# Kernel tuning notes

Hardware: AMD Instinct MI355X
Metric: run time of the kernel (lower is better)

Reference implementation:

```python
import jax, jax.numpy as jnp
import numpy as np

TOP_K = 1
N_EXPERTS = 32
ALPHA = 0.001
SCALING = 1.0


def setup_inputs() -> dict:
    key = jax.random.key(0)
    k1, k2 = jax.random.split(key)
    hidden_states = jax.random.normal(k1, (16, 8192, 256), dtype=jnp.float32)
    # kaiming_uniform-ish gate weight, scale irrelevant for correctness check
    weight = jax.random.normal(k2, (32, 256), dtype=jnp.float32) * 0.06
    return {"hidden_states": hidden_states, "weight": weight}


def reference(hidden_states, weight):
    bsz, seq_len, h = hidden_states.shape
    x = hidden_states.reshape(-1, h).astype(jnp.float32)           # [N, h]
    logits = jnp.einsum('nh,eh->ne', x, weight.astype(jnp.float32))  # [N, E]
    scores = jax.nn.softmax(logits, axis=-1)
    # greedy top-k (sorted order fine; torch uses sorted=False but values identical for k=1)
    topk_weight, topk_idx = jax.lax.top_k(scores, TOP_K)            # [N, K]
    topk_weight = topk_weight * SCALING  # norm_topk_prob=False, top_k=1
    # seq_aux loss (training branch, alpha > 0)
    idx_aux = topk_idx.reshape(bsz, seq_len * TOP_K)                # [B, S*K]
    ce = jax.vmap(lambda idx: jnp.zeros((N_EXPERTS,), jnp.float32).at[idx].add(1.0))(idx_aux)
    ce = ce / (seq_len * TOP_K / N_EXPERTS)
    scores_seq = scores.reshape(bsz, seq_len, N_EXPERTS)
    aux_loss = jnp.mean(jnp.sum(ce * jnp.mean(scores_seq, axis=1), axis=1)) * ALPHA
    return topk_idx, topk_weight, aux_loss
```

## Files before the change

### kernel.cpp

```cpp
#include <hip/hip_runtime.h>
#include <math.h>

#define NTOK (16 * 8192)
#define H    256
#define E    32
#define SEQ  8192
#define BSZ  16

__global__ __launch_bounds__(256) void zero_ws_kernel(float* ws) {
    int i = blockIdx.x * 256 + threadIdx.x;
    if (i < BSZ * E * 2) ws[i] = 0.0f;
}

__global__ __launch_bounds__(256, 2) void gate_kernel(
    const float* __restrict__ x, const float* __restrict__ w,
    float* __restrict__ out, float* __restrict__ ws_cnt, float* __restrict__ ws_sum)
{
    __shared__ float w_lds[E * H];

    const int tid   = threadIdx.x;
    const int token = blockIdx.x * 256 + tid;
    const int lane  = tid & 63;

    {
        float4*       wl = (float4*)w_lds;
        const float4* wg = (const float4*)w;
#pragma unroll
        for (int i = 0; i < (E * H / 4) / 256; ++i)
            wl[tid + 256 * i] = wg[tid + 256 * i];
    }
    __syncthreads();

    float acc[E];
#pragma unroll
    for (int e = 0; e < E; ++e) acc[e] = 0.0f;

    const float* xrow = x + (size_t)token * H;

    float4 cur[4], nxt[4];
#pragma unroll
    for (int j = 0; j < 4; ++j)
        cur[j] = *(const float4*)(xrow + 4 * j);

#pragma unroll 1
    for (int h = 0; h < H; h += 16) {
        const int hn = (h + 16) & (H - 1);
#pragma unroll
        for (int j = 0; j < 4; ++j)
            nxt[j] = *(const float4*)(xrow + hn + 4 * j);

#pragma unroll
        for (int e = 0; e < E; ++e) {
            const float4* wp = (const float4*)(w_lds + e * H + h);
            float s = 0.0f;
#pragma unroll
            for (int j = 0; j < 4; ++j) {
                float4 wv = wp[j];
                s += cur[j].x * wv.x + cur[j].y * wv.y + cur[j].z * wv.z + cur[j].w * wv.w;
            }
            acc[e] += s;
        }
#pragma unroll
        for (int j = 0; j < 4; ++j) cur[j] = nxt[j];
    }

    float m = acc[0];
    int   idx = 0;
#pragma unroll
    for (int e = 1; e < E; ++e) {
        if (acc[e] > m) { m = acc[e]; idx = e; }
    }
    float sc[E];
    float ssum = 0.0f;
#pragma unroll
    for (int e = 0; e < E; ++e) {
        sc[e] = expf(acc[e] - m);
        ssum += sc[e];
    }
    const float inv = 1.0f / ssum;

    out[token]        = (float)idx;
    out[NTOK + token] = inv;

    const int b = token / SEQ;

#pragma unroll 1
    for (int e = 0; e < E; ++e) {
        unsigned long long ball = __ballot(idx == e);
        if (lane == 0 && ball)
            atomicAdd(&ws_cnt[b * E + e], (float)__popcll(ball));
        float v = sc[e] * inv;
#pragma unroll
        for (int off = 32; off > 0; off >>= 1)
            v += __shfl_xor(v, off, 64);
        if (lane == 0)
            atomicAdd(&ws_sum[b * E + e], v);
    }
}

__global__ __launch_bounds__(256) void aux_kernel(
    const float* __restrict__ ws_cnt, const float* __restrict__ ws_sum,
    float* __restrict__ out)
{
    const int tid = threadIdx.x;
    float p = 0.0f;
    for (int i = tid; i < BSZ * E; i += 256)
        p += ws_cnt[i] * ws_sum[i];

    __shared__ float red[4];
#pragma unroll
    for (int off = 32; off > 0; off >>= 1)
        p += __shfl_xor(p, off, 64);
    if ((tid & 63) == 0) red[tid >> 6] = p;
    __syncthreads();
    if (tid == 0) {
        float t = red[0] + red[1] + red[2] + red[3];
        out[2 * NTOK] = t * (0.001f / (16.0f * 256.0f * 8192.0f));
    }
}

extern "C" void kernel_launch(void* const* d_in, const int* in_sizes, int n_in,
                              void* d_out, int out_size, void* d_ws, size_t ws_size,
                              hipStream_t stream) {
    const float* x = (const float*)d_in[0];
    const float* w = (const float*)d_in[1];
    float* out    = (float*)d_out;
    float* ws     = (float*)d_ws;
    float* ws_cnt = ws;
    float* ws_sum = ws + BSZ * E;

    zero_ws_kernel<<<4, 256, 0, stream>>>(ws);
    gate_kernel<<<NTOK / 256, 256, 0, stream>>>(x, w, out, ws_cnt, ws_sum);
    aux_kernel<<<1, 256, 0, stream>>>(ws_cnt, ws_sum, out);
}
```

Before: 284.9 us.

## Compute four tokens per thread with split-K halves to reuse LDS weights

Each thread now accumulates logits for 4 tokens over half of the hidden dimension, so every weight float4 read from LDS is reused across 4 tokens instead of one. The two halves of a wave are combined with a cross-lane shuffle. Each half-lane then finishes softmax and argmax for 2 tokens, and the count and score reductions are merged into one shuffle loop. Blocks shrink to 128 threads while each still covers 256 tokens. The aim is to cut LDS bandwidth per FMA, at the cost of a 128-entry accumulator that raises register pressure and less coalesced global loads, since each lane reads rows spaced H apart.

New measurement: 272.7 us. -4.3%, faster.

```diff
diff --git a/kernel.cpp b/kernel.cpp
--- a/kernel.cpp
+++ b/kernel.cpp
@@ -6,95 +6,116 @@
 #define E    32
 #define SEQ  8192
 #define BSZ  16
+#define T    4
 
 __global__ __launch_bounds__(256) void zero_ws_kernel(float* ws) {
     int i = blockIdx.x * 256 + threadIdx.x;
     if (i < BSZ * E * 2) ws[i] = 0.0f;
 }
 
-__global__ __launch_bounds__(256, 2) void gate_kernel(
+__global__ __launch_bounds__(128, 2) void gate_kernel(
     const float* __restrict__ x, const float* __restrict__ w,
     float* __restrict__ out, float* __restrict__ ws_cnt, float* __restrict__ ws_sum)
 {
     __shared__ float w_lds[E * H];
 
-    const int tid   = threadIdx.x;
-    const int token = blockIdx.x * 256 + tid;
-    const int lane  = tid & 63;
+    const int tid = threadIdx.x;
 
     {
         float4*       wl = (float4*)w_lds;
         const float4* wg = (const float4*)w;
 #pragma unroll
-        for (int i = 0; i < (E * H / 4) / 256; ++i)
-            wl[tid + 256 * i] = wg[tid + 256 * i];
+        for (int i = 0; i < (E * H / 4) / 128; ++i)
+            wl[tid + 128 * i] = wg[tid + 128 * i];
     }
     __syncthreads();
 
-    float acc[E];
+    const int lane = tid & 63;
+    const int col  = lane & 31;
+    const int half = lane >> 5;
+    const int wavebase = blockIdx.x * 256 + (tid >> 6) * 128;
+    const int tok0 = wavebase + col * T;
+
+    const float* xbase = x + (size_t)tok0 * H + half * 128;
+
+    float acc[E][T];
 #pragma unroll
-    for (int e = 0; e < E; ++e) acc[e] = 0.0f;
+    for (int e = 0; e < E; ++e)
+#pragma unroll
+        for (int t = 0; t < T; ++t) acc[e][t] = 0.0f;
 
-    const float* xrow = x + (size_t)token * H;
-
-    float4 cur[4], nxt[4];
+    float4 cur[T], nxt[T];
 #pragma unroll
-    for (int j = 0; j < 4; ++j)
-        cur[j] = *(const float4*)(xrow + 4 * j);
+    for (int t = 0; t < T; ++t)
+        cur[t] = *(const float4*)(xbase + t * H);
 
 #pragma unroll 1
-    for (int h = 0; h < H; h += 16) {
-        const int hn = (h + 16) & (H - 1);
+    for (int hc = 0; hc < 128; hc += 4) {
+        const int hn = (hc + 4) & 127;
 #pragma unroll
-        for (int j = 0; j < 4; ++j)
-            nxt[j] = *(const float4*)(xrow + hn + 4 * j);
+        for (int t = 0; t < T; ++t)
+            nxt[t] = *(const float4*)(xbase + t * H + hn);
 
 #pragma unroll
         for (int e = 0; e < E; ++e) {
-            const float4* wp = (const float4*)(w_lds + e * H + h);
-            float s = 0.0f;
+            const float4 wv = *(const float4*)(w_lds + e * H + half * 128 + hc);
 #pragma unroll
-            for (int j = 0; j < 4; ++j) {
-                float4 wv = wp[j];
-                s += cur[j].x * wv.x + cur[j].y * wv.y + cur[j].z * wv.z + cur[j].w * wv.w;
+            for (int t = 0; t < T; ++t) {
+                acc[e][t] += wv.x * cur[t].x + wv.y * cur[t].y
+                           + wv.z * cur[t].z + wv.w * cur[t].w;
             }
-            acc[e] += s;
         }
 #pragma unroll
-        for (int j = 0; j < 4; ++j) cur[j] = nxt[j];
+        for (int t = 0; t < T; ++t) cur[t] = nxt[t];
     }
 
-    float m = acc[0];
-    int   idx = 0;
 #pragma unroll
-    for (int e = 1; e < E; ++e) {
-        if (acc[e] > m) { m = acc[e]; idx = e; }
+    for (int e = 0; e < E; ++e)
+#pragma unroll
+        for (int t = 0; t < T; ++t)
+            acc[e][t] += __shfl_xor(acc[e][t], 32, 64);
+
+    float m_s[2], inv_s[2];
+    int   idx_s[2];
+#pragma unroll
+    for (int s = 0; s < 2; ++s) {
+        float m = half ? acc[0][2 + s] : acc[0][s];
+        int   id = 0;
+#pragma unroll
+        for (int e = 1; e < E; ++e) {
+            const float v = half ? acc[e][2 + s] : acc[e][s];
+            if (v > m) { m = v; id = e; }
+        }
+        float ss = 0.0f;
+#pragma unroll
+        for (int e = 0; e < E; ++e) {
+            const float v = half ? acc[e][2 + s] : acc[e][s];
+            ss += expf(v - m);
+        }
+        const float inv = 1.0f / ss;
+        const int token = tok0 + half * 2 + s;
+        out[token]        = (float)id;
+        out[NTOK + token] = inv;
+        m_s[s] = m; inv_s[s] = inv; idx_s[s] = id;
     }
-    float sc[E];
-    float ssum = 0.0f;
-#pragma unroll
-    for (int e = 0; e < E; ++e) {
-        sc[e] = expf(acc[e] - m);
-        ssum += sc[e];
-    }
-    const float inv = 1.0f / ssum;
 
-    out[token]        = (float)idx;
-    out[NTOK + token] = inv;
-
-    const int b = token / SEQ;
+    const int b = wavebase >> 13;
 
 #pragma unroll 1
     for (int e = 0; e < E; ++e) {
-        unsigned long long ball = __ballot(idx == e);
-        if (lane == 0 && ball)
-            atomicAdd(&ws_cnt[b * E + e], (float)__popcll(ball));
-        float v = sc[e] * inv;
+        const float v0 = half ? acc[e][2] : acc[e][0];
+        const float v1 = half ? acc[e][3] : acc[e][1];
+        float sc = expf(v0 - m_s[0]) * inv_s[0] + expf(v1 - m_s[1]) * inv_s[1];
+        float cn = (float)((idx_s[0] == e) + (idx_s[1] == e));
 #pragma unroll
-        for (int off = 32; off > 0; off >>= 1)
-            v += __shfl_xor(v, off, 64);
-        if (lane == 0)
-            atomicAdd(&ws_sum[b * E + e], v);
+        for (int off = 32; off > 0; off >>= 1) {
+            sc += __shfl_xor(sc, off, 64);
+            cn += __shfl_xor(cn, off, 64);
+        }
+        if (lane == 0) {
+            atomicAdd(&ws_sum[b * E + e], sc);
+            if (cn != 0.0f) atomicAdd(&ws_cnt[b * E + e], cn);
+        }
     }
 }
 
@@ -130,6 +151,6 @@
     float* ws_sum = ws + BSZ * E;
 
     zero_ws_kernel<<<4, 256, 0, stream>>>(ws);
-    gate_kernel<<<NTOK / 256, 256, 0, stream>>>(x, w, out, ws_cnt, ws_sum);
+    gate_kernel<<<NTOK / 256, 128, 0, stream>>>(x, w, out, ws_cnt, ws_sum);
     aux_kernel<<<1, 256, 0, stream>>>(ws_cnt, ws_sum, out);
 }
```

## Retile gate GEMM into 64-token blocks with LDS-staged x and register tiles

Applied to the files above, without the earlier changes.

Each block now handles 64 tokens instead of 256. Threads split the work across expert groups (8 experts per wave) and hidden-dimension quarters, with x chunks staged through double-buffered LDS and a 4x8 register tile per thread. The softmax max and sum are combined across waves through LDS, and the counts and score sums are reduced with shuffles plus atomics. The aim is fewer per-thread strided row reads, better coalescing and more reuse of weight loads, at the cost of extra syncs, more atomics per token and the 32 KB weight reload now happening in four times as many blocks.

Measured after the change: 297.0 us. +4.2%, slower.

```diff
diff --git a/kernel.cpp b/kernel.cpp
--- a/kernel.cpp
+++ b/kernel.cpp
@@ -6,95 +6,140 @@
 #define E    32
 #define SEQ  8192
 #define BSZ  16
+#define TOKB 64
+#define NCH  16
 
 __global__ __launch_bounds__(256) void zero_ws_kernel(float* ws) {
     int i = blockIdx.x * 256 + threadIdx.x;
     if (i < BSZ * E * 2) ws[i] = 0.0f;
 }
 
-__global__ __launch_bounds__(256, 2) void gate_kernel(
+__global__ __launch_bounds__(256, 4) void gate_kernel(
     const float* __restrict__ x, const float* __restrict__ w,
     float* __restrict__ out, float* __restrict__ ws_cnt, float* __restrict__ ws_sum)
 {
-    __shared__ float w_lds[E * H];
+    __shared__ float  w_lds[E * H];
+    __shared__ float4 xb4[2][256];
 
-    const int tid   = threadIdx.x;
-    const int token = blockIdx.x * 256 + tid;
-    const int lane  = tid & 63;
+    const int tid  = threadIdx.x;
+    const int lane = tid & 63;
+    const int eg   = tid >> 6;
+    const int tg   = lane & 15;
+    const int hq   = lane >> 4;
+
+    const int blkbase = blockIdx.x * TOKB;
 
     {
+        const float4* wg = (const float4*)w;
         float4*       wl = (float4*)w_lds;
-        const float4* wg = (const float4*)w;
 #pragma unroll
-        for (int i = 0; i < (E * H / 4) / 256; ++i)
-            wl[tid + 256 * i] = wg[tid + 256 * i];
+        for (int i = 0; i < 8; ++i) wl[tid + 256 * i] = wg[tid + 256 * i];
+    }
+
+    const int s_tok = tid >> 2, s_part = tid & 3;
+    const float* gsrc = x + (size_t)(blkbase + s_tok) * H + s_part * 4;
+    float4 v = *(const float4*)gsrc;
+
+    float acc[4][8];
+#pragma unroll
+    for (int t = 0; t < 4; ++t)
+#pragma unroll
+        for (int e = 0; e < 8; ++e) acc[t][e] = 0.0f;
+
+#pragma unroll 1
+    for (int kc = 0; kc < NCH; ++kc) {
+        xb4[kc & 1][tid] = v;
+        if (kc < NCH - 1) v = *(const float4*)(gsrc + (kc + 1) * 16);
+        __syncthreads();
+
+        const float* xc = (const float*)xb4[kc & 1];
+        float4 xf[4];
+#pragma unroll
+        for (int t = 0; t < 4; ++t)
+            xf[t] = *(const float4*)(xc + (tg * 4 + t) * 16 + hq * 4);
+
+#pragma unroll
+        for (int e = 0; e < 8; ++e) {
+            const float4 wf = *(const float4*)(w_lds + (eg * 8 + e) * H + kc * 16 + hq * 4);
+#pragma unroll
+            for (int t = 0; t < 4; ++t)
+                acc[t][e] += wf.x * xf[t].x + wf.y * xf[t].y
+                           + wf.z * xf[t].z + wf.w * xf[t].w;
+        }
     }
     __syncthreads();
 
-    float acc[E];
 #pragma unroll
-    for (int e = 0; e < E; ++e) acc[e] = 0.0f;
+    for (int t = 0; t < 4; ++t)
+#pragma unroll
+        for (int e = 0; e < 8; ++e) {
+            acc[t][e] += __shfl_xor(acc[t][e], 16, 64);
+            acc[t][e] += __shfl_xor(acc[t][e], 32, 64);
+        }
 
-    const float* xrow = x + (size_t)token * H;
+    const int etok = tg * 4 + hq;
+    float l[8];
+#pragma unroll
+    for (int e = 0; e < 8; ++e)
+        l[e] = hq == 0 ? acc[0][e] : (hq == 1 ? acc[1][e] : (hq == 2 ? acc[2][e] : acc[3][e]));
 
-    float4 cur[4], nxt[4];
+    float m8 = l[0];
+    int   i8 = 0;
 #pragma unroll
-    for (int j = 0; j < 4; ++j)
-        cur[j] = *(const float4*)(xrow + 4 * j);
+    for (int e = 1; e < 8; ++e)
+        if (l[e] > m8) { m8 = l[e]; i8 = e; }
+    float s8 = 0.0f;
+#pragma unroll
+    for (int e = 0; e < 8; ++e) s8 += expf(l[e] - m8);
 
+    float4* pm = (float4*)xb4;
+    float2* mi = (float2*)((float*)xb4 + 1024);
+    pm[eg * 64 + etok] = make_float4(m8, s8, (float)(eg * 8 + i8), 0.0f);
+    __syncthreads();
+
+    if (tid < 64) {
+        const int tok = tid;
+        float4 p[4];
+#pragma unroll
+        for (int g = 0; g < 4; ++g) p[g] = pm[g * 64 + tok];
+
+        float M = p[0].x, idxf = p[0].z;
+#pragma unroll
+        for (int g = 1; g < 4; ++g)
+            if (p[g].x > M) { M = p[g].x; idxf = p[g].z; }
+        float S = 0.0f;
+#pragma unroll
+        for (int g = 0; g < 4; ++g) S += p[g].y * expf(p[g].x - M);
+        const float inv = 1.0f / S;
+
+        const int T = blkbase + tok;
+        out[T]        = idxf;
+        out[NTOK + T] = inv;
+        mi[tok] = make_float2(M, inv);
+
+        const int IDX = (int)idxf;
+        const int b   = T >> 13;
 #pragma unroll 1
-    for (int h = 0; h < H; h += 16) {
-        const int hn = (h + 16) & (H - 1);
+        for (int e = 0; e < E; ++e) {
+            unsigned long long ball = __ballot(IDX == e);
+            if (lane == 0 && ball)
+                atomicAdd(&ws_cnt[b * E + e], (float)__popcll(ball));
+        }
+    }
+    __syncthreads();
+
+    {
+        const float2 p = mi[etok];
+        const int b = blkbase >> 13;
+#pragma unroll 1
+        for (int e = 0; e < 8; ++e) {
+            float sc = expf(l[e] - p.x) * p.y;
 #pragma unroll
-        for (int j = 0; j < 4; ++j)
-            nxt[j] = *(const float4*)(xrow + hn + 4 * j);
-
-#pragma unroll
-        for (int e = 0; e < E; ++e) {
-            const float4* wp = (const float4*)(w_lds + e * H + h);
-            float s = 0.0f;
-#pragma unroll
-            for (int j = 0; j < 4; ++j) {
-                float4 wv = wp[j];
-                s += cur[j].x * wv.x + cur[j].y * wv.y + cur[j].z * wv.z + cur[j].w * wv.w;
-            }
-            acc[e] += s;
+            for (int off = 32; off > 0; off >>= 1)
+                sc += __shfl_xor(sc, off, 64);
+            if (lane == 0)
+                atomicAdd(&ws_sum[b * E + eg * 8 + e], sc);
         }
-#pragma unroll
-        for (int j = 0; j < 4; ++j) cur[j] = nxt[j];
-    }
-
-    float m = acc[0];
-    int   idx = 0;
-#pragma unroll
-    for (int e = 1; e < E; ++e) {
-        if (acc[e] > m) { m = acc[e]; idx = e; }
-    }
-    float sc[E];
-    float ssum = 0.0f;
-#pragma unroll
-    for (int e = 0; e < E; ++e) {
-        sc[e] = expf(acc[e] - m);
-        ssum += sc[e];
-    }
-    const float inv = 1.0f / ssum;
-
-    out[token]        = (float)idx;
-    out[NTOK + token] = inv;
-
-    const int b = token / SEQ;
-
-#pragma unroll 1
-    for (int e = 0; e < E; ++e) {
-        unsigned long long ball = __ballot(idx == e);
-        if (lane == 0 && ball)
-            atomicAdd(&ws_cnt[b * E + e], (float)__popcll(ball));
-        float v = sc[e] * inv;
-#pragma unroll
-        for (int off = 32; off > 0; off >>= 1)
-            v += __shfl_xor(v, off, 64);
-        if (lane == 0)
-            atomicAdd(&ws_sum[b * E + e], v);
     }
 }
 
@@ -130,6 +175,6 @@
     float* ws_sum = ws + BSZ * E;
 
     zero_ws_kernel<<<4, 256, 0, stream>>>(ws);
-    gate_kernel<<<NTOK / 256, 256, 0, stream>>>(x, w, out, ws_cnt, ws_sum);
+    gate_kernel<<<NTOK / TOKB, 256, 0, stream>>>(x, w, out, ws_cnt, ws_sum);
     aux_kernel<<<1, 256, 0, stream>>>(ws_cnt, ws_sum, out);
 }
```
